# Performance work log

Hardware: AMD Instinct MI355X
Metric: run time of the kernel (lower is better)

Reference implementation:

```python
import jax, jax.numpy as jnp
import numpy as np


def setup_inputs() -> dict:
    key = jax.random.key(0)
    k1, k2, k3 = jax.random.split(key, 3)
    B, R, Din, D = 4096, 4096, 1024, 1024
    x = jax.random.normal(k1, (B, Din), dtype=jnp.float32)
    refs = jax.random.normal(k2, (R, Din), dtype=jnp.float32)
    W = jax.random.normal(k3, (Din, D), dtype=jnp.float32) * (1.0 / np.sqrt(Din))
    b = jnp.zeros((D,), dtype=jnp.float32)
    return {"x": x, "refs": refs, "W": W, "b": b}


def reference(x, refs, W, b) -> jnp.ndarray:
    # feature extractor (linear stand-in for the CResNet embedding)
    vin = x @ W + b          # (B, D)
    vrefs = refs @ W + b     # (R, D)
    # compute_degradation_metric: mean_r ||vin_b - vref_r||^2
    # = ||vin||^2 + mean_r ||vref_r||^2 - 2 * vin @ mean_r(vref_r)
    # Same math as the naive broadcast-sub-square-sum-mean, GEMM-friendly form.
    sq_in = jnp.sum(vin * vin, axis=1)                 # (B,)
    mean_sq_ref = jnp.mean(jnp.sum(vrefs * vrefs, axis=1))  # scalar
    mean_ref = jnp.mean(vrefs, axis=0)                 # (D,)
    cross = vin @ mean_ref                             # (B,)
    degradation_metric = sq_in + mean_sq_ref - 2.0 * cross
    return degradation_metric
```

## Files before the change

kernel.cpp:

```cpp
#include <hip/hip_runtime.h>
#include <hip/hip_bf16.h>
#include <stdint.h>


typedef __attribute__((ext_vector_type(8))) short short8;
typedef __attribute__((ext_vector_type(4))) float f32x4;

__device__ __forceinline__ short f2bf(float f) {
  uint32_t u = __builtin_bit_cast(uint32_t, f);
  uint32_t r = (u + 0x7fffu + ((u >> 16) & 1u)) >> 16;
  return (short)r;
}
__device__ __forceinline__ float bf2f(short s) {
  uint32_t u = ((uint32_t)(uint16_t)s) << 16;
  return __builtin_bit_cast(float, u);
}

#define WS_XB 0u
#define WS_RB 8388608u
#define WS_WT 16777216u
#define WS_CP 18874368u
#define WS_CS 20971520u
#define WS_TV 20975616u
#define WS_XP 20979712u
#define WS_RR 20996096u

__global__ __launch_bounds__(256) void k_prep(
    const float* __restrict__ x, const float* __restrict__ refs,
    const float* __restrict__ W, short* __restrict__ xb, short* __restrict__ rb,
    short* __restrict__ wt, float* __restrict__ cspart, float* __restrict__ zacc) {
  __shared__ short tile[64][68];
  const int b = blockIdx.x, t = threadIdx.x;
  if (b < 512) {
    for (int i = b * 256 + t; i < 1048576; i += 512 * 256) {
      float4 v = ((const float4*)x)[i];
      uint32_t lo = (uint16_t)f2bf(v.x) | ((uint32_t)(uint16_t)f2bf(v.y) << 16);
      uint32_t hi = (uint16_t)f2bf(v.z) | ((uint32_t)(uint16_t)f2bf(v.w) << 16);
      ((uint2*)xb)[i] = make_uint2(lo, hi);
    }
  } else if (b < 1024) {
    const int rblk = b - 512;
    const int c0 = t * 4;
    float s0 = 0.f, s1 = 0.f, s2 = 0.f, s3 = 0.f;
    for (int r = rblk * 8; r < rblk * 8 + 8; ++r) {
      float4 v = *(const float4*)&refs[(size_t)r * 1024 + c0];
      s0 += v.x; s1 += v.y; s2 += v.z; s3 += v.w;
      uint32_t lo = (uint16_t)f2bf(v.x) | ((uint32_t)(uint16_t)f2bf(v.y) << 16);
      uint32_t hi = (uint16_t)f2bf(v.z) | ((uint32_t)(uint16_t)f2bf(v.w) << 16);
      *(uint2*)&rb[(size_t)r * 1024 + c0] = make_uint2(lo, hi);
    }
    cspart[rblk * 1024 + c0 + 0] = s0;
    cspart[rblk * 1024 + c0 + 1] = s1;
    cspart[rblk * 1024 + c0 + 2] = s2;
    cspart[rblk * 1024 + c0 + 3] = s3;
  } else if (b < 1280) {
    const int tb = b - 1024;
    const int tk = (tb >> 4) * 64, tn = (tb & 15) * 64;
    const int kk = t >> 4, nn4 = (t & 15) * 4;
#pragma unroll
    for (int p = 0; p < 4; ++p) {
      int k = kk + p * 16;
      float4 v = *(const float4*)&W[(size_t)(tk + k) * 1024 + tn + nn4];
      tile[nn4 + 0][k] = f2bf(v.x);
      tile[nn4 + 1][k] = f2bf(v.y);
      tile[nn4 + 2][k] = f2bf(v.z);
      tile[nn4 + 3][k] = f2bf(v.w);
    }
    __syncthreads();
    const int nn = t >> 4, kk4 = (t & 15) * 4;
#pragma unroll
    for (int p = 0; p < 4; ++p) {
      int n = nn + p * 16;
      uint32_t lo = (uint16_t)tile[n][kk4 + 0] | ((uint32_t)(uint16_t)tile[n][kk4 + 1] << 16);
      uint32_t hi = (uint16_t)tile[n][kk4 + 2] | ((uint32_t)(uint16_t)tile[n][kk4 + 3] << 16);
      *(uint2*)&wt[(size_t)(tn + n) * 1024 + tk + kk4] = make_uint2(lo, hi);
    }
  } else {
    const int i = (b - 1280) * 256 + t;
    ((float4*)zacc)[i]        = make_float4(0.f, 0.f, 0.f, 0.f);
    ((float4*)zacc)[i + 1024] = make_float4(0.f, 0.f, 0.f, 0.f);
  }
}

__global__ void k_colsum(const float* __restrict__ cspart, float* __restrict__ colsum) {
  __shared__ float sh[8][32];
  const int t = threadIdx.x;
  const int c = t & 31, pg = t >> 5;
  const int k = blockIdx.x * 32 + c;
  float s = 0.f;
  for (int i = 0; i < 64; ++i) s += cspart[(size_t)(pg * 64 + i) * 1024 + k];
  sh[pg][c] = s;
  __syncthreads();
  if (t < 32) {
    float tot = 0.f;
#pragma unroll
    for (int g = 0; g < 8; ++g) tot += sh[g][t];
    colsum[blockIdx.x * 32 + t] = tot;
  }
}

__global__ void k_tvec(const short* __restrict__ Wt, const float* __restrict__ colsum,
                       const float* __restrict__ bias, float* __restrict__ tv) {
  int w = threadIdx.x >> 6, l = threadIdx.x & 63;
  int n = blockIdx.x * 4 + w;
  float s = 0.f;
  for (int k = l; k < 1024; k += 64)
    s += colsum[k] * (1.0f / 4096.0f) * bf2f(Wt[(size_t)n * 1024 + k]);
#pragma unroll
  for (int off = 32; off; off >>= 1) s += __shfl_down(s, off, 64);
  if (l == 0) tv[n] = s + bias[n];
}

__global__ __launch_bounds__(256) void k_main(
    const short* __restrict__ Xb, const short* __restrict__ Rb,
    const short* __restrict__ Wt, const float* __restrict__ bias,
    const float* __restrict__ tv, float* __restrict__ xpart,
    float* __restrict__ refrow) {
  __shared__ __align__(16) short As[2][128 * 64];
  __shared__ __align__(16) short Bs[2][128 * 64];
  const int t = threadIdx.x;
  const int w = t >> 6, l = t & 63;
  const int wr = w >> 1, wc = w & 1;
  const int bx = blockIdx.x;
  const int nt = bx & 7;
  const int mt = bx >> 3;
  const bool is_x = (mt < 32);
  const short* Am = is_x ? Xb : Rb;
  const int m0 = (is_x ? mt : (mt - 32)) * 128;
  const int n0 = nt * 128;

  const int srow = t >> 3;
  const int sslot = t & 7;

  f32x4 acc[4][4] = {};

  auto stage = [&](int buf, int kt) {
    const int k0 = kt * 64;
#pragma unroll
    for (int issue = 0; issue < 4; ++issue) {
      const int row = srow + issue * 32;
      const int sg = sslot ^ (row & 7);
      const short* ga = Am + ((size_t)(m0 + row) * 1024 + k0 + sg * 8);
      const short* gb = Wt + ((size_t)(n0 + row) * 1024 + k0 + sg * 8);
      char* la = (char*)&As[buf][0] + issue * 4096 + w * 1024;
      char* lb = (char*)&Bs[buf][0] + issue * 4096 + w * 1024;
      __builtin_amdgcn_global_load_lds(
          (const __attribute__((address_space(1))) unsigned int*)ga,
          (__attribute__((address_space(3))) unsigned int*)la, 16, 0, 0);
      __builtin_amdgcn_global_load_lds(
          (const __attribute__((address_space(1))) unsigned int*)gb,
          (__attribute__((address_space(3))) unsigned int*)lb, 16, 0, 0);
    }
  };

  stage(0, 0);
  asm volatile("s_waitcnt vmcnt(0)" ::: "memory");
  __builtin_amdgcn_s_barrier();

  int cur = 0;
  for (int kt = 0; kt < 16; ++kt) {
    if (kt < 15) stage(cur ^ 1, kt + 1);
#pragma unroll
    for (int kk = 0; kk < 2; ++kk) {
      short8 af[4], bfr[4];
#pragma unroll
      for (int i = 0; i < 4; ++i) {
        const int ra = wr * 64 + i * 16 + (l & 15);
        const int rbw = wc * 64 + i * 16 + (l & 15);
        const int s = (l >> 4) + kk * 4;
        af[i]  = *(const short8*)&As[cur][ra * 64 + ((s ^ (ra & 7)) * 8)];
        bfr[i] = *(const short8*)&Bs[cur][rbw * 64 + ((s ^ (rbw & 7)) * 8)];
      }
#pragma unroll
      for (int i = 0; i < 4; ++i)
#pragma unroll
        for (int j2 = 0; j2 < 4; ++j2)
          acc[i][j2] = __builtin_amdgcn_mfma_f32_16x16x32_bf16(af[i], bfr[j2], acc[i][j2], 0, 0, 0);
    }
    asm volatile("s_waitcnt vmcnt(0)" ::: "memory");
    __builtin_amdgcn_s_barrier();
    cur ^= 1;
  }

  float bv[4], tvv[4];
#pragma unroll
  for (int n4 = 0; n4 < 4; ++n4) {
    const int col = n0 + wc * 64 + n4 * 16 + (l & 15);
    bv[n4] = bias[col];
    tvv[n4] = tv[col];
  }
#pragma unroll
  for (int m4 = 0; m4 < 4; ++m4) {
#pragma unroll
    for (int j = 0; j < 4; ++j) {
      float sq = 0.f, cr = 0.f;
#pragma unroll
      for (int n4 = 0; n4 < 4; ++n4) {
        const float v = acc[m4][n4][j] + bv[n4];
        sq += v * v;
        cr += v * tvv[n4];
      }
#pragma unroll
      for (int off = 1; off < 16; off <<= 1) {
        sq += __shfl_xor(sq, off, 64);
        cr += __shfl_xor(cr, off, 64);
      }
      if ((l & 15) == 0) {
        const int rm = m0 + wr * 64 + m4 * 16 + (l >> 4) * 4 + j;
        if (is_x) atomicAdd(&xpart[rm], sq - 2.0f * cr);
        else      atomicAdd(&refrow[rm], sq);
      }
    }
  }
}

__global__ void k_tail(const float* __restrict__ refrow, const float* __restrict__ xpart,
                       float* __restrict__ out) {
  __shared__ float sh[16];
  const int t = threadIdx.x;
  float s = 0.f;
  for (int i = t; i < 4096; i += 1024) s += refrow[i];
#pragma unroll
  for (int off = 32; off; off >>= 1) s += __shfl_down(s, off, 64);
  const int w = t >> 6, l = t & 63;
  if (l == 0) sh[w] = s;
  __syncthreads();
  if (t == 0) {
    float tot = 0.f;
#pragma unroll
    for (int i = 0; i < 16; ++i) tot += sh[i];
    sh[0] = tot * (1.0f / 4096.0f);
  }
  __syncthreads();
  const float ms = sh[0];
  for (int i = t; i < 4096; i += 1024) out[i] = xpart[i] + ms;
}

extern "C" void kernel_launch(void* const* d_in, const int* in_sizes, int n_in,
                              void* d_out, int out_size, void* d_ws, size_t ws_size,
                              hipStream_t stream) {
  const float* x    = (const float*)d_in[0];
  const float* refs = (const float*)d_in[1];
  const float* W    = (const float*)d_in[2];
  const float* bias = (const float*)d_in[3];
  float* out = (float*)d_out;
  char* ws = (char*)d_ws;

  short* xb     = (short*)(ws + WS_XB);
  short* rb     = (short*)(ws + WS_RB);
  short* wt     = (short*)(ws + WS_WT);
  float* cspart = (float*)(ws + WS_CP);
  float* colsum = (float*)(ws + WS_CS);
  float* tvv    = (float*)(ws + WS_TV);
  float* xpart  = (float*)(ws + WS_XP);
  float* refrow = (float*)(ws + WS_RR);

  hipLaunchKernelGGL(k_prep, dim3(1284), dim3(256), 0, stream, x, refs, W, xb, rb, wt, cspart, xpart);
  hipLaunchKernelGGL(k_colsum, dim3(32), dim3(256), 0, stream, cspart, colsum);
  hipLaunchKernelGGL(k_tvec, dim3(256), dim3(256), 0, stream, wt, colsum, bias, tvv);
  hipLaunchKernelGGL(k_main, dim3(512), dim3(256), 0, stream, xb, rb, wt, bias, tvv, xpart, refrow);
  hipLaunchKernelGGL(k_tail, dim3(1), dim3(1024), 0, stream, refrow, xpart, out);
}
```

Before: 55.26 us.

## Fuse tvec computation into main GEMM and deepen LDS prefetch pipeline

Removes the separate k_tvec launch. Each main-kernel block now computes the 128 entries of the projected mean-reference vector for its column tile, overlapped with the first two async LDS stages, and keeps bias and tvec in LDS. The k-loop is restructured to keep two stages in flight, using partial vmcnt waits and issuing the next load after the compute barrier. It also raises wave priority around the MFMA blocks. The trade-off is that every block redundantly reads 128 rows of Wt for tvec, 8x total redundancy across the M tiles.

```diff
diff --git a/kernel.cpp b/kernel.cpp
--- a/kernel.cpp
+++ b/kernel.cpp
@@ -21,7 +21,6 @@
 #define WS_WT 16777216u
 #define WS_CP 18874368u
 #define WS_CS 20971520u
-#define WS_TV 20975616u
 #define WS_XP 20979712u
 #define WS_RR 20996096u
 
@@ -99,25 +98,15 @@
   }
 }
 
-__global__ void k_tvec(const short* __restrict__ Wt, const float* __restrict__ colsum,
-                       const float* __restrict__ bias, float* __restrict__ tv) {
-  int w = threadIdx.x >> 6, l = threadIdx.x & 63;
-  int n = blockIdx.x * 4 + w;
-  float s = 0.f;
-  for (int k = l; k < 1024; k += 64)
-    s += colsum[k] * (1.0f / 4096.0f) * bf2f(Wt[(size_t)n * 1024 + k]);
-#pragma unroll
-  for (int off = 32; off; off >>= 1) s += __shfl_down(s, off, 64);
-  if (l == 0) tv[n] = s + bias[n];
-}
-
 __global__ __launch_bounds__(256) void k_main(
     const short* __restrict__ Xb, const short* __restrict__ Rb,
     const short* __restrict__ Wt, const float* __restrict__ bias,
-    const float* __restrict__ tv, float* __restrict__ xpart,
+    const float* __restrict__ colsum, float* __restrict__ xpart,
     float* __restrict__ refrow) {
   __shared__ __align__(16) short As[2][128 * 64];
   __shared__ __align__(16) short Bs[2][128 * 64];
+  __shared__ float tlds[128], blds[128];
+  __shared__ float tpart[128][2];
   const int t = threadIdx.x;
   const int w = t >> 6, l = t & 63;
   const int wr = w >> 1, wc = w & 1;
@@ -154,12 +143,33 @@
   };
 
   stage(0, 0);
-  asm volatile("s_waitcnt vmcnt(0)" ::: "memory");
-  __builtin_amdgcn_s_barrier();
-
-  int cur = 0;
+  stage(1, 1);
+  {
+    const int n_off = t & 127, half = t >> 7;
+    const short* wrow = Wt + (size_t)(n0 + n_off) * 1024 + half * 512;
+    const float* cs = colsum + half * 512;
+    float s = 0.f;
+    for (int i = 0; i < 64; ++i) {
+      short8 wv = *(const short8*)(wrow + i * 8);
+      float4 c0 = *(const float4*)(cs + i * 8);
+      float4 c1 = *(const float4*)(cs + i * 8 + 4);
+      s += c0.x * bf2f(wv[0]) + c0.y * bf2f(wv[1]) + c0.z * bf2f(wv[2]) + c0.w * bf2f(wv[3])
+         + c1.x * bf2f(wv[4]) + c1.y * bf2f(wv[5]) + c1.z * bf2f(wv[6]) + c1.w * bf2f(wv[7]);
+    }
+    tpart[n_off][half] = s * (1.0f / 4096.0f);
+  }
+  __syncthreads();
+  if (t < 128) {
+    const float bv = bias[n0 + t];
+    blds[t] = bv;
+    tlds[t] = tpart[t][0] + tpart[t][1] + bv;
+  }
+
   for (int kt = 0; kt < 16; ++kt) {
-    if (kt < 15) stage(cur ^ 1, kt + 1);
+    if (kt < 15) asm volatile("s_waitcnt vmcnt(8)" ::: "memory");
+    else         asm volatile("s_waitcnt vmcnt(0)" ::: "memory");
+    __builtin_amdgcn_s_barrier();
+    const int cur = kt & 1;
 #pragma unroll
     for (int kk = 0; kk < 2; ++kk) {
       short8 af[4], bfr[4];
@@ -171,23 +181,24 @@
         af[i]  = *(const short8*)&As[cur][ra * 64 + ((s ^ (ra & 7)) * 8)];
         bfr[i] = *(const short8*)&Bs[cur][rbw * 64 + ((s ^ (rbw & 7)) * 8)];
       }
+      __builtin_amdgcn_s_setprio(1);
 #pragma unroll
       for (int i = 0; i < 4; ++i)
 #pragma unroll
         for (int j2 = 0; j2 < 4; ++j2)
           acc[i][j2] = __builtin_amdgcn_mfma_f32_16x16x32_bf16(af[i], bfr[j2], acc[i][j2], 0, 0, 0);
-    }
-    asm volatile("s_waitcnt vmcnt(0)" ::: "memory");
+      __builtin_amdgcn_s_setprio(0);
+    }
     __builtin_amdgcn_s_barrier();
-    cur ^= 1;
+    if (kt + 2 < 16) stage(cur, kt + 2);
   }
 
   float bv[4], tvv[4];
 #pragma unroll
   for (int n4 = 0; n4 < 4; ++n4) {
-    const int col = n0 + wc * 64 + n4 * 16 + (l & 15);
-    bv[n4] = bias[col];
-    tvv[n4] = tv[col];
+    const int ci = wc * 64 + n4 * 16 + (l & 15);
+    bv[n4] = blds[ci];
+    tvv[n4] = tlds[ci];
   }
 #pragma unroll
   for (int m4 = 0; m4 < 4; ++m4) {
@@ -251,13 +262,11 @@
   short* wt     = (short*)(ws + WS_WT);
   float* cspart = (float*)(ws + WS_CP);
   float* colsum = (float*)(ws + WS_CS);
-  float* tvv    = (float*)(ws + WS_TV);
   float* xpart  = (float*)(ws + WS_XP);
   float* refrow = (float*)(ws + WS_RR);
 
   hipLaunchKernelGGL(k_prep, dim3(1284), dim3(256), 0, stream, x, refs, W, xb, rb, wt, cspart, xpart);
   hipLaunchKernelGGL(k_colsum, dim3(32), dim3(256), 0, stream, cspart, colsum);
-  hipLaunchKernelGGL(k_tvec, dim3(256), dim3(256), 0, stream, wt, colsum, bias, tvv);
-  hipLaunchKernelGGL(k_main, dim3(512), dim3(256), 0, stream, xb, rb, wt, bias, tvv, xpart, refrow);
+  hipLaunchKernelGGL(k_main, dim3(512), dim3(256), 0, stream, xb, rb, wt, bias, colsum, xpart, refrow);
   hipLaunchKernelGGL(k_tail, dim3(1), dim3(1024), 0, stream, refrow, xpart, out);
 }
```

Result: slower. 68.52 us (+24.0%).

## Use 8 waves per GEMM block with deeper load-ahead pipeline and MFMA priority

Applied to the files above, without the earlier changes.

The main GEMM kernel goes from 256 to 512 threads per block. Each wave now computes a 64x32 sub-tile instead of 64x64, which halves accumulator registers and B-fragment loads per wave. The staging loop is restructured so two K-tiles are in flight, with a partial vmcnt wait, and the freed buffer is refilled after the compute barrier. s_setprio is raised around the MFMA bursts. The aim is more latency hiding and occupancy, at the cost of more A-fragment LDS reads per MFMA and an extra barrier per iteration.

```diff
diff --git a/kernel.cpp b/kernel.cpp
--- a/kernel.cpp
+++ b/kernel.cpp
@@ -111,7 +111,7 @@
   if (l == 0) tv[n] = s + bias[n];
 }
 
-__global__ __launch_bounds__(256) void k_main(
+__global__ __launch_bounds__(512) void k_main(
     const short* __restrict__ Xb, const short* __restrict__ Rb,
     const short* __restrict__ Wt, const float* __restrict__ bias,
     const float* __restrict__ tv, float* __restrict__ xpart,
@@ -120,7 +120,7 @@
   __shared__ __align__(16) short Bs[2][128 * 64];
   const int t = threadIdx.x;
   const int w = t >> 6, l = t & 63;
-  const int wr = w >> 1, wc = w & 1;
+  const int wr = w >> 2, wc = w & 3;
   const int bx = blockIdx.x;
   const int nt = bx & 7;
   const int mt = bx >> 3;
@@ -132,18 +132,18 @@
   const int srow = t >> 3;
   const int sslot = t & 7;
 
-  f32x4 acc[4][4] = {};
+  f32x4 acc[4][2] = {};
 
   auto stage = [&](int buf, int kt) {
     const int k0 = kt * 64;
 #pragma unroll
-    for (int issue = 0; issue < 4; ++issue) {
-      const int row = srow + issue * 32;
+    for (int issue = 0; issue < 2; ++issue) {
+      const int row = srow + issue * 64;
       const int sg = sslot ^ (row & 7);
       const short* ga = Am + ((size_t)(m0 + row) * 1024 + k0 + sg * 8);
       const short* gb = Wt + ((size_t)(n0 + row) * 1024 + k0 + sg * 8);
-      char* la = (char*)&As[buf][0] + issue * 4096 + w * 1024;
-      char* lb = (char*)&Bs[buf][0] + issue * 4096 + w * 1024;
+      char* la = (char*)&As[buf][0] + issue * 8192 + w * 1024;
+      char* lb = (char*)&Bs[buf][0] + issue * 8192 + w * 1024;
       __builtin_amdgcn_global_load_lds(
           (const __attribute__((address_space(1))) unsigned int*)ga,
           (__attribute__((address_space(3))) unsigned int*)la, 16, 0, 0);
@@ -154,40 +154,46 @@
   };
 
   stage(0, 0);
-  asm volatile("s_waitcnt vmcnt(0)" ::: "memory");
-  __builtin_amdgcn_s_barrier();
-
-  int cur = 0;
+  stage(1, 1);
+
   for (int kt = 0; kt < 16; ++kt) {
-    if (kt < 15) stage(cur ^ 1, kt + 1);
+    if (kt < 15) asm volatile("s_waitcnt vmcnt(4)" ::: "memory");
+    else         asm volatile("s_waitcnt vmcnt(0)" ::: "memory");
+    __builtin_amdgcn_s_barrier();
+    const int cur = kt & 1;
 #pragma unroll
     for (int kk = 0; kk < 2; ++kk) {
-      short8 af[4], bfr[4];
+      short8 af[4], bfr[2];
 #pragma unroll
       for (int i = 0; i < 4; ++i) {
         const int ra = wr * 64 + i * 16 + (l & 15);
-        const int rbw = wc * 64 + i * 16 + (l & 15);
         const int s = (l >> 4) + kk * 4;
-        af[i]  = *(const short8*)&As[cur][ra * 64 + ((s ^ (ra & 7)) * 8)];
-        bfr[i] = *(const short8*)&Bs[cur][rbw * 64 + ((s ^ (rbw & 7)) * 8)];
-      }
+        af[i] = *(const short8*)&As[cur][ra * 64 + ((s ^ (ra & 7)) * 8)];
+      }
+#pragma unroll
+      for (int j = 0; j < 2; ++j) {
+        const int rbw = wc * 32 + j * 16 + (l & 15);
+        const int s = (l >> 4) + kk * 4;
+        bfr[j] = *(const short8*)&Bs[cur][rbw * 64 + ((s ^ (rbw & 7)) * 8)];
+      }
+      __builtin_amdgcn_s_setprio(1);
 #pragma unroll
       for (int i = 0; i < 4; ++i)
 #pragma unroll
-        for (int j2 = 0; j2 < 4; ++j2)
-          acc[i][j2] = __builtin_amdgcn_mfma_f32_16x16x32_bf16(af[i], bfr[j2], acc[i][j2], 0, 0, 0);
-    }
-    asm volatile("s_waitcnt vmcnt(0)" ::: "memory");
+        for (int j = 0; j < 2; ++j)
+          acc[i][j] = __builtin_amdgcn_mfma_f32_16x16x32_bf16(af[i], bfr[j], acc[i][j], 0, 0, 0);
+      __builtin_amdgcn_s_setprio(0);
+    }
     __builtin_amdgcn_s_barrier();
-    cur ^= 1;
-  }
-
-  float bv[4], tvv[4];
-#pragma unroll
-  for (int n4 = 0; n4 < 4; ++n4) {
-    const int col = n0 + wc * 64 + n4 * 16 + (l & 15);
-    bv[n4] = bias[col];
-    tvv[n4] = tv[col];
+    if (kt + 2 < 16) stage(cur, kt + 2);
+  }
+
+  float bv[2], tvv[2];
+#pragma unroll
+  for (int n2 = 0; n2 < 2; ++n2) {
+    const int col = n0 + wc * 32 + n2 * 16 + (l & 15);
+    bv[n2] = bias[col];
+    tvv[n2] = tv[col];
   }
 #pragma unroll
   for (int m4 = 0; m4 < 4; ++m4) {
@@ -195,10 +201,10 @@
     for (int j = 0; j < 4; ++j) {
       float sq = 0.f, cr = 0.f;
 #pragma unroll
-      for (int n4 = 0; n4 < 4; ++n4) {
-        const float v = acc[m4][n4][j] + bv[n4];
+      for (int n2 = 0; n2 < 2; ++n2) {
+        const float v = acc[m4][n2][j] + bv[n2];
         sq += v * v;
-        cr += v * tvv[n4];
+        cr += v * tvv[n2];
       }
 #pragma unroll
       for (int off = 1; off < 16; off <<= 1) {
@@ -258,6 +264,6 @@
   hipLaunchKernelGGL(k_prep, dim3(1284), dim3(256), 0, stream, x, refs, W, xb, rb, wt, cspart, xpart);
   hipLaunchKernelGGL(k_colsum, dim3(32), dim3(256), 0, stream, cspart, colsum);
   hipLaunchKernelGGL(k_tvec, dim3(256), dim3(256), 0, stream, wt, colsum, bias, tvv);
-  hipLaunchKernelGGL(k_main, dim3(512), dim3(256), 0, stream, xb, rb, wt, bias, tvv, xpart, refrow);
+  hipLaunchKernelGGL(k_main, dim3(512), dim3(512), 0, stream, xb, rb, wt, bias, tvv, xpart, refrow);
   hipLaunchKernelGGL(k_tail, dim3(1), dim3(1024), 0, stream, refrow, xpart, out);
 }
```

After: 55.26 us. Within noise of the previous version (+0.0%).
